# Optimization experiments

Hardware: AMD Instinct MI355X
Metric: run time of the kernel (lower is better)

The kernel has to match this reference:

```python
import jax, jax.numpy as jnp
import numpy as np

D_MODEL, D_STATE, D_CONV, EXPAND = 1024, 16, 4, 2
D_INNER = EXPAND * D_MODEL
B, L = 4, 2048


def setup_inputs() -> dict:
    key = jax.random.key(0)
    ks = jax.random.split(key, 9)
    s = lambda fan_in: 1.0 / np.sqrt(fan_in)
    x = jax.random.normal(ks[0], (B, L, D_MODEL), dtype=jnp.float32)
    W_in = jax.random.normal(ks[1], (D_MODEL, 2 * D_INNER), dtype=jnp.float32) * s(D_MODEL)
    conv_w = jax.random.normal(ks[2], (D_INNER, 1, D_CONV), dtype=jnp.float32) * s(D_CONV)
    conv_b = jax.random.normal(ks[3], (D_INNER,), dtype=jnp.float32) * 0.01
    W_x = jax.random.normal(ks[4], (D_INNER, 2 * D_STATE + 1), dtype=jnp.float32) * s(D_INNER)
    W_dt = jax.random.normal(ks[5], (1, D_INNER), dtype=jnp.float32)
    b_dt = jax.random.normal(ks[6], (D_INNER,), dtype=jnp.float32) * 0.01
    A_log = jnp.log(jnp.tile(jnp.arange(1, D_STATE + 1, dtype=jnp.float32), (D_INNER, 1)))
    D_param = jnp.ones((D_INNER,), dtype=jnp.float32)
    W_out = jax.random.normal(ks[7], (D_INNER, D_MODEL), dtype=jnp.float32) * s(D_INNER)
    return {"x": x, "W_in": W_in, "conv_w": conv_w, "conv_b": conv_b, "W_x": W_x,
            "W_dt": W_dt, "b_dt": b_dt, "A_log": A_log, "D_param": D_param, "W_out": W_out}


def _mamba_forward(x, W_in, conv_w, conv_b, W_x, W_dt, b_dt, A_log, D_param, W_out):
    b, l, _ = x.shape
    xz = x @ W_in                      # [B,L,2*D_INNER]
    x_in, z = jnp.split(xz, 2, axis=-1)
    # causal depthwise conv1d (padding=d_conv-1 on the left, trimmed to L)
    xc = jnp.transpose(x_in, (0, 2, 1))  # [B,C,L]
    xc = jax.lax.conv_general_dilated(
        xc, conv_w, window_strides=(1,), padding=[(D_CONV - 1, 0)],
        dimension_numbers=("NCH", "OIH", "NCH"), feature_group_count=D_INNER)
    xc = xc + conv_b[None, :, None]
    x_conv = jax.nn.silu(jnp.transpose(xc, (0, 2, 1)))  # [B,L,D_INNER]

    xp = x_conv @ W_x                  # [B,L,1+2*D_STATE]
    delta1, B_mat, C_mat = jnp.split(xp, [1, 1 + D_STATE], axis=-1)
    delta = jax.nn.softplus(delta1 @ W_dt + b_dt)       # [B,L,D_INNER]
    A = -jnp.exp(A_log)                # [D_INNER,D_STATE]

    # selective scan over time
    def step(h, inp):
        d_t, B_t, C_t, x_t = inp       # [B,Di], [B,Ds], [B,Ds], [B,Di]
        A_bar = jnp.exp(d_t[:, :, None] * A)                       # [B,Di,Ds]
        h = A_bar * h + (d_t * x_t)[:, :, None] * B_t[:, None, :]  # [B,Di,Ds]
        y = jnp.einsum("bds,bs->bd", h, C_t)                        # [B,Di]
        return h, y

    h0 = jnp.zeros((b, D_INNER, D_STATE), dtype=x.dtype)
    tm = lambda a: jnp.transpose(a, (1, 0, 2))  # time-major
    _, ys = jax.lax.scan(step, h0, (tm(delta), tm(B_mat), tm(C_mat), tm(x_conv)))
    y = jnp.transpose(ys, (1, 0, 2))   # [B,L,D_INNER]

    y = y + x_conv * D_param
    y = y * jax.nn.silu(z)
    return y @ W_out                   # [B,L,D_MODEL]


def reference(x, W_in, conv_w, conv_b, W_x, W_dt, b_dt, A_log, D_param, W_out):
    return _mamba_forward(x, W_in, conv_w, conv_b, W_x, W_dt, b_dt, A_log, D_param, W_out)
```

## Files before the change

kernel.cpp:

```cpp
#include <hip/hip_runtime.h>
#include <hip/hip_bf16.h>
#include <stdint.h>

#define D_STATE 16
#define D_INNER 2048
#define BB 4
#define LL 2048
#define NTOK (BB*LL)
#define NCH 32
#define CHUNK (LL/NCH)
#define XPW 48
#define SCAN_TPB 128

typedef __attribute__((ext_vector_type(8))) short short8;
typedef __attribute__((ext_vector_type(8))) unsigned short u16x8;
typedef __attribute__((ext_vector_type(4))) float f32x4;
typedef __attribute__((ext_vector_type(2))) float f32x2;

__device__ __forceinline__ float b2f(__hip_bfloat16 v) { return __bfloat162float(v); }
__device__ __forceinline__ float ub2f(unsigned short u) {
  unsigned v = (unsigned)u << 16; float f; __builtin_memcpy(&f, &v, 4); return f;
}

__device__ __forceinline__ void g2lds16(const void* g, void* l) {
  __builtin_amdgcn_global_load_lds(
      (const __attribute__((address_space(1))) unsigned*)(uintptr_t)g,
      (__attribute__((address_space(3))) unsigned*)(unsigned)(uintptr_t)l,
      16, 0, 0);
}

__device__ __forceinline__ void store_c(float* p, float v) { *p = v; }
__device__ __forceinline__ void store_c(__hip_bfloat16* p, float v) { *p = __float2bfloat16(v); }

#define PREP_B0 8192
#define PREP_B1 (PREP_B0 + 4096)
#define PREP_B2 (PREP_B1 + 2048)
#define PREP_B3 (PREP_B2 + 384)
__global__ __launch_bounds__(256) void prep_kernel(
    const float* __restrict__ x, __hip_bfloat16* __restrict__ xb,
    const float* __restrict__ W_in, __hip_bfloat16* __restrict__ WT_in,
    const float* __restrict__ W_out, __hip_bfloat16* __restrict__ WT_out,
    const float* __restrict__ W_x, __hip_bfloat16* __restrict__ WTx)
{
  __shared__ float tile[32][33];
  const int bx = blockIdx.x, tid = threadIdx.x;
  if (bx < PREP_B0) {
    int i = bx * 256 + tid;
    const float4 v = ((const float4*)x)[i];
    __hip_bfloat16 o[4] = { __float2bfloat16(v.x), __float2bfloat16(v.y),
                            __float2bfloat16(v.z), __float2bfloat16(v.w) };
    ((ulong1*)xb)[i] = *(ulong1*)o;
  } else if (bx < PREP_B2) {
    const float* in; __hip_bfloat16* out; int R, C, tc, tr;
    if (bx < PREP_B1) {
      int tb = bx - PREP_B0; in = W_in; out = WT_in; R = 1024; C = 4096;
      tc = (tb & 127) * 32; tr = (tb >> 7) * 32;
    } else {
      int tb = bx - PREP_B1; in = W_out; out = WT_out; R = 2048; C = 1024;
      tc = (tb & 31) * 32; tr = (tb >> 5) * 32;
    }
    const int lx = tid & 31, ly = tid >> 5;
    #pragma unroll
    for (int i = 0; i < 32; i += 8)
      tile[ly + i][lx] = in[(size_t)(tr + ly + i) * C + tc + lx];
    __syncthreads();
    #pragma unroll
    for (int i = 0; i < 32; i += 8)
      out[(size_t)(tc + ly + i) * R + tr + lx] = __float2bfloat16(tile[lx][ly + i]);
  } else {
    int idx = (bx - PREP_B2) * 256 + tid;
    int n = idx >> 11, k = idx & 2047;
    int src = (n == 0) ? 0 : ((n >= 2 && n <= 33) ? n - 1 : -1);
    float v = (src >= 0) ? W_x[k * 33 + src] : 0.f;
    WTx[idx] = __float2bfloat16(v);
  }
}

__global__ __launch_bounds__(512, 2) void gemm_bt_256(
    const short* __restrict__ A, const short* __restrict__ BT,
    __hip_bfloat16* __restrict__ C)
{
  constexpr int K = 1024, Nstride = 4096, nk = K >> 5;
  __shared__ alignas(16) short As[4][256 * 32];
  __shared__ alignas(16) short Bs[4][256 * 32];
  const int tid = threadIdx.x;
  const int lane = tid & 63, wid = tid >> 6;
  const int wm = wid & 1, wn = wid >> 1;
  const int lrow = lane & 15, lq = lane >> 4;

  const int wg = blockIdx.x;
  const int xcd = wg & 7, j = wg >> 3;
  const int jm = j >> 2, jn = j & 3;
  const int m0 = ((xcd >> 2) * 16 + jm) * 256;
  const int n0 = ((xcd & 3) * 4 + jn) * 256;

  const int i0 = tid, i1 = tid + 512;
  const int r0 = i0 >> 2, r1 = i1 >> 2;
  const int sw0 = ((i0 & 3) ^ ((r0 >> 1) & 3)) * 8;
  const int sw1 = ((i1 & 3) ^ ((r1 >> 1) & 3)) * 8;
  const short* pA0 = A  + (size_t)(m0 + r0) * K + sw0;
  const short* pA1 = A  + (size_t)(m0 + r1) * K + sw1;
  const short* pB0 = BT + (size_t)(n0 + r0) * K + sw0;
  const short* pB1 = BT + (size_t)(n0 + r1) * K + sw1;

  int offA[8], offB[4];
  #pragma unroll
  for (int mi = 0; mi < 8; ++mi) {
    int ra = wm * 128 + mi * 16 + lrow;
    offA[mi] = ra * 32 + (lq ^ ((ra >> 1) & 3)) * 8;
  }
  #pragma unroll
  for (int ni = 0; ni < 4; ++ni) {
    int rb = wn * 64 + ni * 16 + lrow;
    offB[ni] = rb * 32 + (lq ^ ((rb >> 1) & 3)) * 8;
  }

  f32x4 acc[8][4] = {};
  short8 a0[4], b0[4];

  auto stageA = [&](int t) {
    const int k0 = t << 5, slot = t & 3;
    g2lds16(pA0 + k0, &As[slot][i0 * 8]);
    g2lds16(pA1 + k0, &As[slot][i1 * 8]);
  };
  auto stageB = [&](int t) {
    const int k0 = t << 5, slot = t & 3;
    g2lds16(pB0 + k0, &Bs[slot][i0 * 8]);
    g2lds16(pB1 + k0, &Bs[slot][i1 * 8]);
  };

  auto body = [&](int t, bool doStage, bool doAhead, bool vm4, bool doBar) {
    const int slot = t & 3, slot2 = (t + 1) & 3;
    const short* as = &As[slot][0];
    const short* bs = &Bs[slot][0];
    short8 a1[4];
    #pragma unroll
    for (int mi = 0; mi < 4; ++mi) a1[mi] = *(const short8*)(as + offA[4 + mi]);
    if (doStage) stageA(t + 3);
    __builtin_amdgcn_s_setprio(1);
    #pragma unroll
    for (int mi = 0; mi < 4; ++mi)
      #pragma unroll
      for (int ni = 0; ni < 4; ++ni)
        acc[mi][ni] = __builtin_amdgcn_mfma_f32_16x16x32_bf16(
            a0[mi], b0[ni], acc[mi][ni], 0, 0, 0);
    __builtin_amdgcn_s_setprio(0);
    if (doStage) stageB(t + 3);
    short8 an[4], bn[4];
    if (doAhead) {
      const short* as2 = &As[slot2][0];
      const short* bs2 = &Bs[slot2][0];
      #pragma unroll
      for (int mi = 0; mi < 4; ++mi) an[mi] = *(const short8*)(as2 + offA[mi]);
      #pragma unroll
      for (int ni = 0; ni < 4; ++ni) bn[ni] = *(const short8*)(bs2 + offB[ni]);
    }
    __builtin_amdgcn_s_setprio(1);
    #pragma unroll
    for (int mi = 0; mi < 4; ++mi)
      #pragma unroll
      for (int ni = 0; ni < 4; ++ni)
        acc[4 + mi][ni] = __builtin_amdgcn_mfma_f32_16x16x32_bf16(
            a1[mi], b0[ni], acc[4 + mi][ni], 0, 0, 0);
    __builtin_amdgcn_s_setprio(0);
    if (doAhead) {
      #pragma unroll
      for (int i = 0; i < 4; ++i) { a0[i] = an[i]; b0[i] = bn[i]; }
    }
    if (doBar) {
      if (vm4) asm volatile("s_waitcnt vmcnt(4)\n\ts_barrier" ::: "memory");
      else     asm volatile("s_waitcnt vmcnt(0)\n\ts_barrier" ::: "memory");
    }
  };

  stageA(0); stageB(0); stageA(1); stageB(1); stageA(2); stageB(2);
  asm volatile("s_waitcnt vmcnt(4)\n\ts_barrier" ::: "memory");
  #pragma unroll
  for (int mi = 0; mi < 4; ++mi) a0[mi] = *(const short8*)(&As[0][offA[mi]]);
  #pragma unroll
  for (int ni = 0; ni < 4; ++ni) b0[ni] = *(const short8*)(&Bs[0][offB[ni]]);

  #pragma unroll 4
  for (int t = 0; t < nk - 4; ++t)
    body(t, true, true, true, true);
  body(nk - 4, true,  true,  true,  true);
  body(nk - 3, false, true,  false, true);
  body(nk - 2, false, true,  false, false);
  body(nk - 1, false, false, false, false);

  #pragma unroll
  for (int mi = 0; mi < 8; ++mi)
    #pragma unroll
    for (int ni = 0; ni < 4; ++ni) {
      const int col = n0 + wn * 64 + ni * 16 + lrow;
      #pragma unroll
      for (int r = 0; r < 4; ++r) {
        const int rowg = m0 + wm * 128 + mi * 16 + lq * 4 + r;
        C[(size_t)rowg * Nstride + col] = __float2bfloat16(acc[mi][ni][r]);
      }
    }
}

template <typename OT>
__global__ __launch_bounds__(256) void gemm_bt_128(
    const short* __restrict__ A, const short* __restrict__ BT,
    OT* __restrict__ C, int Nstride, int K)
{
  __shared__ alignas(16) short As[2][128 * 32];
  __shared__ alignas(16) short Bs[2][128 * 32];
  const int tid = threadIdx.x;
  const int lane = tid & 63, wid = tid >> 6;
  const int wm = wid & 1, wn = wid >> 1;
  const int lrow = lane & 15, lq = lane >> 4;

  const int wg = blockIdx.x;
  const int xcd = wg & 7, j = wg >> 3;
  const int jm = j >> 3, jn = j & 7;
  const int m0 = (xcd * 8 + jm) * 128;
  const int n0 = jn * 128;

  f32x4 acc[4][4] = {};

  auto stage = [&](int k0, int buf) {
    #pragma unroll
    for (int t = 0; t < 2; ++t) {
      int idx = t * 256 + tid;
      int row = idx >> 2, kq = idx & 3;
      int ksw = (kq ^ ((row >> 1) & 3)) * 8;
      g2lds16(A  + (size_t)(m0 + row) * K + k0 + ksw, &As[buf][idx * 8]);
      g2lds16(BT + (size_t)(n0 + row) * K + k0 + ksw, &Bs[buf][idx * 8]);
    }
  };

  const int nk = K >> 5;
  stage(0, 0);
  for (int ki = 0; ki < nk; ++ki) {
    const int cur = ki & 1;
    if (ki + 1 < nk) {
      stage((ki + 1) << 5, cur ^ 1);
      asm volatile("s_waitcnt vmcnt(4)\n\ts_barrier" ::: "memory");
    } else {
      asm volatile("s_waitcnt vmcnt(0)\n\ts_barrier" ::: "memory");
    }

    short8 af[4], bfr[4];
    #pragma unroll
    for (int i = 0; i < 4; ++i) {
      int ra = wm * 64 + i * 16 + lrow;
      int rb = wn * 64 + i * 16 + lrow;
      af[i]  = *(const short8*)(&As[cur][ra * 32 + (lq ^ ((ra >> 1) & 3)) * 8]);
      bfr[i] = *(const short8*)(&Bs[cur][rb * 32 + (lq ^ ((rb >> 1) & 3)) * 8]);
    }
    #pragma unroll
    for (int mi = 0; mi < 4; ++mi)
      #pragma unroll
      for (int ni = 0; ni < 4; ++ni)
        acc[mi][ni] = __builtin_amdgcn_mfma_f32_16x16x32_bf16(
            af[mi], bfr[ni], acc[mi][ni], 0, 0, 0);
    asm volatile("s_barrier" ::: "memory");
  }

  #pragma unroll
  for (int mi = 0; mi < 4; ++mi)
    #pragma unroll
    for (int ni = 0; ni < 4; ++ni) {
      int col = n0 + wn * 64 + ni * 16 + lrow;
      #pragma unroll
      for (int r = 0; r < 4; ++r) {
        int rowg = m0 + wm * 64 + mi * 16 + lq * 4 + r;
        store_c(&C[(size_t)rowg * Nstride + col], acc[mi][ni][r]);
      }
    }
}

__global__ __launch_bounds__(256) void gemm_xp(
    const short* __restrict__ A, const short* __restrict__ BT,
    float* __restrict__ Cout)
{
  __shared__ alignas(16) short As[2][64 * 32];
  __shared__ alignas(16) short Bs[2][48 * 32];
  const int tid = threadIdx.x;
  const int lane = tid & 63, wid = tid >> 6;
  const int lrow = lane & 15, lq = lane >> 4;
  const int m0 = blockIdx.x * 64;
  const int row = tid >> 2, kq = tid & 3;
  const int ksw = (kq ^ ((row >> 1) & 3)) * 8;
  const short* pA = A  + (size_t)(m0 + row) * 2048 + ksw;
  const short* pB = BT + (size_t)row * 2048 + ksw;

  f32x4 acc[3] = {};

  auto stage = [&](int k0, int buf) {
    g2lds16(pA + k0, &As[buf][tid * 8]);
    if (wid < 3) g2lds16(pB + k0, &Bs[buf][tid * 8]);
  };

  stage(0, 0);
  for (int ki = 0; ki < 64; ++ki) {
    const int cur = ki & 1;
    if (ki < 63) {
      stage((ki + 1) << 5, cur ^ 1);
      if (wid < 3) asm volatile("s_waitcnt vmcnt(2)\n\ts_barrier" ::: "memory");
      else         asm volatile("s_waitcnt vmcnt(1)\n\ts_barrier" ::: "memory");
    } else {
      asm volatile("s_waitcnt vmcnt(0)\n\ts_barrier" ::: "memory");
    }
    int ra = wid * 16 + lrow;
    short8 af = *(const short8*)(&As[cur][ra * 32 + (lq ^ ((ra >> 1) & 3)) * 8]);
    #pragma unroll
    for (int nt = 0; nt < 3; ++nt) {
      int rb = nt * 16 + lrow;
      short8 bfr = *(const short8*)(&Bs[cur][rb * 32 + (lq ^ ((rb >> 1) & 3)) * 8]);
      acc[nt] = __builtin_amdgcn_mfma_f32_16x16x32_bf16(af, bfr, acc[nt], 0, 0, 0);
    }
    asm volatile("s_barrier" ::: "memory");
  }
  #pragma unroll
  for (int nt = 0; nt < 3; ++nt) {
    int col = nt * 16 + lrow;
    #pragma unroll
    for (int r = 0; r < 4; ++r) {
      int rowg = m0 + wid * 16 + lq * 4 + r;
      Cout[(size_t)rowg * XPW + col] = acc[nt][r];
    }
  }
}

__global__ __launch_bounds__(256) void conv_silu(
    const __hip_bfloat16* __restrict__ xz, const float* __restrict__ conv_w,
    const float* __restrict__ conv_b, __hip_bfloat16* __restrict__ x_conv)
{
  const int t0 = (blockIdx.x & 255) * 8;
  const int b  = blockIdx.x >> 8;
  const int d8 = threadIdx.x * 8;

  float cb[8];
  {
    float4 cb0 = *(const float4*)(conv_b + d8);
    float4 cb1 = *(const float4*)(conv_b + d8 + 4);
    cb[0] = cb0.x; cb[1] = cb0.y; cb[2] = cb0.z; cb[3] = cb0.w;
    cb[4] = cb1.x; cb[5] = cb1.y; cb[6] = cb1.z; cb[7] = cb1.w;
  }
  float4 w[8];
  #pragma unroll
  for (int j = 0; j < 8; ++j) w[j] = *(const float4*)(conv_w + (size_t)(d8 + j) * 4);

  u16x8 xv[11];
  #pragma unroll
  for (int k = 0; k < 11; ++k) {
    int tt = t0 - 3 + k;
    if (tt >= 0)
      xv[k] = *(const u16x8*)(xz + (size_t)(b * LL + tt) * 4096 + d8);
    else
      xv[k] = (u16x8){0, 0, 0, 0, 0, 0, 0, 0};
  }

  #pragma unroll
  for (int j = 0; j < 8; ++j) {
    float acc[8];
    #pragma unroll
    for (int c = 0; c < 8; ++c) acc[c] = cb[c];
    #pragma unroll
    for (int k = 0; k < 4; ++k) {
      #pragma unroll
      for (int c = 0; c < 8; ++c) {
        float wk = (k == 0) ? w[c].x : (k == 1) ? w[c].y : (k == 2) ? w[c].z : w[c].w;
        acc[c] = fmaf(wk, ub2f(xv[j + k][c]), acc[c]);
      }
    }
    __hip_bfloat16 o[8];
    #pragma unroll
    for (int c = 0; c < 8; ++c) {
      float r = acc[c] * __builtin_amdgcn_rcpf(1.f + __expf(-acc[c]));
      o[c] = __float2bfloat16(r);
    }
    *(u16x8*)(x_conv + (size_t)(b * LL + t0 + j) * D_INNER + d8) = *(u16x8*)o;
  }
}


__global__ __launch_bounds__(SCAN_TPB) void scan_phase1(
    const float* __restrict__ xp, const __hip_bfloat16* __restrict__ x_conv,
    const float* __restrict__ W_dt, const float* __restrict__ b_dt,
    float* __restrict__ P1b, float* __restrict__ vb)
{
  const int d = blockIdx.x * SCAN_TPB + threadIdx.x;
  const int c = blockIdx.y, b = blockIdx.z;
  const float Wdt = W_dt[d], bdt = b_dt[d];
  f32x2 v[8];
  #pragma unroll
  for (int i = 0; i < 8; ++i) v[i] = (f32x2){0.f, 0.f};
  float P1 = 1.f;
  const int t0 = c * CHUNK;
  for (int tt = 0; tt < CHUNK; ++tt) {
    const size_t row = (size_t)b * LL + t0 + tt;
    const float* xpt = xp + row * XPW;
    float u = fmaf(xpt[0], Wdt, bdt);
    float e = __expf(u);
    float r = __builtin_amdgcn_rcpf(1.f + e);
    float delta = (u > 20.f) ? u : __logf(1.f + e);
    float du = delta * b2f(x_conv[row * D_INNER + d]);
    float rr = r * r;
    f32x2 a   = {r, rr};
    f32x2 rr2 = {rr, rr};
    f32x2 du2 = {du, du};
    #pragma unroll
    for (int i = 0; i < 8; ++i) {
      f32x2 B2 = *(const f32x2*)(xpt + 2 + 2 * i);
      v[i] = a * v[i] + du2 * B2;
      a = a * rr2;
    }
    P1 *= r;
  }
  const size_t vbase = (size_t)(b * NCH + c) * (D_STATE * D_INNER) + d;
  #pragma unroll
  for (int i = 0; i < 8; ++i) {
    vb[vbase + (size_t)(2 * i)     * D_INNER] = v[i].x;
    vb[vbase + (size_t)(2 * i + 1) * D_INNER] = v[i].y;
  }
  P1b[((size_t)(b * NCH + c) << 11) + d] = P1;
}

__global__ __launch_bounds__(256) void scan_phase2(
    const float* __restrict__ P1b, float* __restrict__ vb)
{
  const int idx = blockIdx.x * 256 + threadIdx.x;
  const int b = idx >> 14, r2 = idx & 16383;
  const int s = r2 >> 10, d2 = r2 & 1023;
  f32x2 h = {0.f, 0.f};
  for (int c = 0; c < NCH; ++c) {
    f32x2 P1 = *(const f32x2*)(P1b + (((size_t)(b * NCH + c)) << 11) + d2 * 2);
    f32x2 P = P1;
    for (int j = 0; j < s; ++j) P *= P1;
    float* vp = vb + (((size_t)(b * NCH + c)) << 15) + (s << 11) + d2 * 2;
    f32x2 v = *(const f32x2*)vp;
    *(f32x2*)vp = h;
    h = P * h + v;
  }
}

__global__ __launch_bounds__(SCAN_TPB) void scan_phase3(
    const float* __restrict__ xp, const __hip_bfloat16* __restrict__ x_conv,
    const __hip_bfloat16* __restrict__ xz,
    const float* __restrict__ W_dt, const float* __restrict__ b_dt,
    const float* __restrict__ D_param,
    const float* __restrict__ hb, __hip_bfloat16* __restrict__ yout)
{
  const int d = blockIdx.x * SCAN_TPB + threadIdx.x;
  const int c = blockIdx.y, b = blockIdx.z;
  const float Wdt = W_dt[d], bdt = b_dt[d];
  const float Dp = D_param[d];
  f32x2 h[8];
  const size_t base = (size_t)(b * NCH + c) * (D_STATE * D_INNER) + d;
  #pragma unroll
  for (int i = 0; i < 8; ++i) {
    h[i].x = hb[base + (size_t)(2 * i)     * D_INNER];
    h[i].y = hb[base + (size_t)(2 * i + 1) * D_INNER];
  }
  const int t0 = c * CHUNK;
  for (int tt = 0; tt < CHUNK; ++tt) {
    const size_t row = (size_t)b * LL + t0 + tt;
    const float* xpt = xp + row * XPW;
    float u = fmaf(xpt[0], Wdt, bdt);
    float e = __expf(u);
    float r = __builtin_amdgcn_rcpf(1.f + e);
    float delta = (u > 20.f) ? u : __logf(1.f + e);
    float xt = b2f(x_conv[row * D_INNER + d]);
    float du = delta * xt;
    float rr = r * r;
    f32x2 a   = {r, rr};
    f32x2 rr2 = {rr, rr};
    f32x2 du2 = {du, du};
    f32x2 y2  = {0.f, 0.f};
    #pragma unroll
    for (int i = 0; i < 8; ++i) {
      f32x2 B2 = *(const f32x2*)(xpt + 2 + 2 * i);
      f32x2 C2 = *(const f32x2*)(xpt + 18 + 2 * i);
      h[i] = a * h[i] + du2 * B2;
      y2 = h[i] * C2 + y2;
      a = a * rr2;
    }
    float y = y2.x + y2.y + xt * Dp;
    float z = b2f(xz[row * 4096 + D_INNER + d]);
    y *= z * __builtin_amdgcn_rcpf(1.f + __expf(-z));
    yout[row * D_INNER + d] = __float2bfloat16(y);
  }
}

extern "C" void kernel_launch(void* const* d_in, const int* in_sizes, int n_in,
                              void* d_out, int out_size, void* d_ws, size_t ws_size,
                              hipStream_t stream) {
  const float* x      = (const float*)d_in[0];
  const float* W_in   = (const float*)d_in[1];
  const float* conv_w = (const float*)d_in[2];
  const float* conv_b = (const float*)d_in[3];
  const float* W_x    = (const float*)d_in[4];
  const float* W_dt   = (const float*)d_in[5];
  const float* b_dt   = (const float*)d_in[6];
  const float* D_par  = (const float*)d_in[8];
  const float* W_out  = (const float*)d_in[9];
  float* out = (float*)d_out;

  char* ws = (char*)d_ws;
  size_t off = 0;
  auto alloc = [&](size_t bytes) -> void* {
    void* p = ws + off; off += (bytes + 255) & ~(size_t)255; return p;
  };
  const size_t SCANB = (size_t)BB * NCH * D_STATE * D_INNER * 4;
  const size_t R1B   = (size_t)NTOK * D_INNER * 2;

  char* R1 = (char*)alloc(R1B);
  __hip_bfloat16* xb    = (__hip_bfloat16*)R1;
  __hip_bfloat16* WT_in = (__hip_bfloat16*)(R1 + (size_t)NTOK * 1024 * 2);
  float* P1b = (float*)R1;
  __hip_bfloat16* y_ws = (__hip_bfloat16*)R1;
  char* R2 = (char*)alloc(SCANB);
  float* vb = (float*)R2;

  __hip_bfloat16* xz     = (__hip_bfloat16*)alloc((size_t)NTOK * 4096 * 2);
  __hip_bfloat16* x_conv = (__hip_bfloat16*)alloc((size_t)NTOK * D_INNER * 2);
  __hip_bfloat16* WT_out = (__hip_bfloat16*)alloc((size_t)1024 * 2048 * 2);
  __hip_bfloat16* WT_x   = (__hip_bfloat16*)alloc((size_t)XPW * 2048 * 2);
  float* xp = (float*)alloc((size_t)NTOK * XPW * 4);
  (void)ws_size; (void)in_sizes; (void)n_in; (void)out_size;

  prep_kernel<<<PREP_B3, 256, 0, stream>>>(x, xb, W_in, WT_in, W_out, WT_out, W_x, WT_x);
  gemm_bt_256<<<512, 512, 0, stream>>>(
      (const short*)xb, (const short*)WT_in, xz);
  conv_silu<<<NTOK / 8, 256, 0, stream>>>(xz, conv_w, conv_b, x_conv);
  gemm_xp<<<NTOK / 64, 256, 0, stream>>>((const short*)x_conv, (const short*)WT_x, xp);
  scan_phase1<<<dim3(D_INNER / SCAN_TPB, NCH, BB), SCAN_TPB, 0, stream>>>(
      xp, x_conv, W_dt, b_dt, P1b, vb);
  scan_phase2<<<(BB * D_STATE * D_INNER / 2) / 256, 256, 0, stream>>>(P1b, vb);
  scan_phase3<<<dim3(D_INNER / SCAN_TPB, NCH, BB), SCAN_TPB, 0, stream>>>(
      xp, x_conv, xz, W_dt, b_dt, D_par, vb, y_ws);
  gemm_bt_128<float><<<512, 256, 0, stream>>>(
      (const short*)y_ws, (const short*)WT_out, out, 1024, 2048);
}
```

Measured before the change: 364.8 us.

## Shrink input GEMM tiles to 256x128 with 3-stage pipeline and higher occupancy

```diff
diff --git a/kernel.cpp b/kernel.cpp
--- a/kernel.cpp
+++ b/kernel.cpp
@@ -76,37 +76,36 @@
   }
 }
 
-__global__ __launch_bounds__(512, 2) void gemm_bt_256(
+__global__ __launch_bounds__(512, 4) void gemm_bt_w(
     const short* __restrict__ A, const short* __restrict__ BT,
     __hip_bfloat16* __restrict__ C)
 {
   constexpr int K = 1024, Nstride = 4096, nk = K >> 5;
-  __shared__ alignas(16) short As[4][256 * 32];
-  __shared__ alignas(16) short Bs[4][256 * 32];
+  __shared__ alignas(16) short As[3][256 * 32];
+  __shared__ alignas(16) short Bs[3][128 * 32];
   const int tid = threadIdx.x;
   const int lane = tid & 63, wid = tid >> 6;
-  const int wm = wid & 1, wn = wid >> 1;
+  const int wm = wid & 3, wn = wid >> 2;
   const int lrow = lane & 15, lq = lane >> 4;
 
   const int wg = blockIdx.x;
   const int xcd = wg & 7, j = wg >> 3;
-  const int jm = j >> 2, jn = j & 3;
+  const int jm = j >> 3, jn = j & 7;
   const int m0 = ((xcd >> 2) * 16 + jm) * 256;
-  const int n0 = ((xcd & 3) * 4 + jn) * 256;
-
-  const int i0 = tid, i1 = tid + 512;
-  const int r0 = i0 >> 2, r1 = i1 >> 2;
-  const int sw0 = ((i0 & 3) ^ ((r0 >> 1) & 3)) * 8;
-  const int sw1 = ((i1 & 3) ^ ((r1 >> 1) & 3)) * 8;
-  const short* pA0 = A  + (size_t)(m0 + r0) * K + sw0;
-  const short* pA1 = A  + (size_t)(m0 + r1) * K + sw1;
-  const short* pB0 = BT + (size_t)(n0 + r0) * K + sw0;
-  const short* pB1 = BT + (size_t)(n0 + r1) * K + sw1;
-
-  int offA[8], offB[4];
-  #pragma unroll
-  for (int mi = 0; mi < 8; ++mi) {
-    int ra = wm * 128 + mi * 16 + lrow;
+  const int n0 = ((xcd & 3) * 8 + jn) * 128;
+
+  const int row0 = tid >> 2, kq = tid & 3;
+  const int row1 = (tid + 512) >> 2;
+  const int sw0 = (kq ^ ((row0 >> 1) & 3)) * 8;
+  const int sw1 = (kq ^ ((row1 >> 1) & 3)) * 8;
+  const short* pA0 = A  + (size_t)(m0 + row0) * K + sw0;
+  const short* pA1 = A  + (size_t)(m0 + row1) * K + sw1;
+  const short* pB0 = BT + (size_t)(n0 + row0) * K + sw0;
+
+  int offA[4], offB[4];
+  #pragma unroll
+  for (int mi = 0; mi < 4; ++mi) {
+    int ra = wm * 64 + mi * 16 + lrow;
     offA[mi] = ra * 32 + (lq ^ ((ra >> 1) & 3)) * 8;
   }
   #pragma unroll
@@ -115,87 +114,56 @@
     offB[ni] = rb * 32 + (lq ^ ((rb >> 1) & 3)) * 8;
   }
 
-  f32x4 acc[8][4] = {};
-  short8 a0[4], b0[4];
-
-  auto stageA = [&](int t) {
-    const int k0 = t << 5, slot = t & 3;
-    g2lds16(pA0 + k0, &As[slot][i0 * 8]);
-    g2lds16(pA1 + k0, &As[slot][i1 * 8]);
+  f32x4 acc[4][4] = {};
+
+  auto stage = [&](int t) {
+    const int k0 = t << 5, slot = t % 3;
+    g2lds16(pA0 + k0, &As[slot][tid * 8]);
+    g2lds16(pA1 + k0, &As[slot][(tid + 512) * 8]);
+    g2lds16(pB0 + k0, &Bs[slot][tid * 8]);
   };
-  auto stageB = [&](int t) {
-    const int k0 = t << 5, slot = t & 3;
-    g2lds16(pB0 + k0, &Bs[slot][i0 * 8]);
-    g2lds16(pB1 + k0, &Bs[slot][i1 * 8]);
-  };
-
-  auto body = [&](int t, bool doStage, bool doAhead, bool vm4, bool doBar) {
-    const int slot = t & 3, slot2 = (t + 1) & 3;
+
+  auto body = [&](int t, bool doStage, int endmode) {
+    const int slot = t % 3;
     const short* as = &As[slot][0];
     const short* bs = &Bs[slot][0];
-    short8 a1[4];
-    #pragma unroll
-    for (int mi = 0; mi < 4; ++mi) a1[mi] = *(const short8*)(as + offA[4 + mi]);
-    if (doStage) stageA(t + 3);
+    short8 af[4], bf[4];
+    #pragma unroll
+    for (int mi = 0; mi < 4; ++mi) af[mi] = *(const short8*)(as + offA[mi]);
+    #pragma unroll
+    for (int ni = 0; ni < 4; ++ni) bf[ni] = *(const short8*)(bs + offB[ni]);
+    if (doStage) stage(t + 2);
     __builtin_amdgcn_s_setprio(1);
     #pragma unroll
     for (int mi = 0; mi < 4; ++mi)
       #pragma unroll
       for (int ni = 0; ni < 4; ++ni)
         acc[mi][ni] = __builtin_amdgcn_mfma_f32_16x16x32_bf16(
-            a0[mi], b0[ni], acc[mi][ni], 0, 0, 0);
+            af[mi], bf[ni], acc[mi][ni], 0, 0, 0);
     __builtin_amdgcn_s_setprio(0);
-    if (doStage) stageB(t + 3);
-    short8 an[4], bn[4];
-    if (doAhead) {
-      const short* as2 = &As[slot2][0];
-      const short* bs2 = &Bs[slot2][0];
-      #pragma unroll
-      for (int mi = 0; mi < 4; ++mi) an[mi] = *(const short8*)(as2 + offA[mi]);
-      #pragma unroll
-      for (int ni = 0; ni < 4; ++ni) bn[ni] = *(const short8*)(bs2 + offB[ni]);
-    }
-    __builtin_amdgcn_s_setprio(1);
-    #pragma unroll
-    for (int mi = 0; mi < 4; ++mi)
-      #pragma unroll
-      for (int ni = 0; ni < 4; ++ni)
-        acc[4 + mi][ni] = __builtin_amdgcn_mfma_f32_16x16x32_bf16(
-            a1[mi], b0[ni], acc[4 + mi][ni], 0, 0, 0);
-    __builtin_amdgcn_s_setprio(0);
-    if (doAhead) {
-      #pragma unroll
-      for (int i = 0; i < 4; ++i) { a0[i] = an[i]; b0[i] = bn[i]; }
-    }
-    if (doBar) {
-      if (vm4) asm volatile("s_waitcnt vmcnt(4)\n\ts_barrier" ::: "memory");
-      else     asm volatile("s_waitcnt vmcnt(0)\n\ts_barrier" ::: "memory");
-    }
+    if (endmode == 3)
+      asm volatile("s_waitcnt vmcnt(3)\n\ts_barrier" ::: "memory");
+    else if (endmode == 0)
+      asm volatile("s_waitcnt vmcnt(0)\n\ts_barrier" ::: "memory");
   };
 
-  stageA(0); stageB(0); stageA(1); stageB(1); stageA(2); stageB(2);
-  asm volatile("s_waitcnt vmcnt(4)\n\ts_barrier" ::: "memory");
-  #pragma unroll
-  for (int mi = 0; mi < 4; ++mi) a0[mi] = *(const short8*)(&As[0][offA[mi]]);
-  #pragma unroll
-  for (int ni = 0; ni < 4; ++ni) b0[ni] = *(const short8*)(&Bs[0][offB[ni]]);
-
-  #pragma unroll 4
-  for (int t = 0; t < nk - 4; ++t)
-    body(t, true, true, true, true);
-  body(nk - 4, true,  true,  true,  true);
-  body(nk - 3, false, true,  false, true);
-  body(nk - 2, false, true,  false, false);
-  body(nk - 1, false, false, false, false);
-
-  #pragma unroll
-  for (int mi = 0; mi < 8; ++mi)
+  stage(0); stage(1);
+  asm volatile("s_waitcnt vmcnt(0)\n\ts_barrier" ::: "memory");
+
+  #pragma unroll 3
+  for (int t = 0; t < nk - 2; ++t)
+    body(t, true, 3);
+  body(nk - 2, false, 0);
+  body(nk - 1, false, -1);
+
+  #pragma unroll
+  for (int mi = 0; mi < 4; ++mi)
     #pragma unroll
     for (int ni = 0; ni < 4; ++ni) {
       const int col = n0 + wn * 64 + ni * 16 + lrow;
       #pragma unroll
       for (int r = 0; r < 4; ++r) {
-        const int rowg = m0 + wm * 128 + mi * 16 + lq * 4 + r;
+        const int rowg = m0 + wm * 64 + mi * 16 + lq * 4 + r;
         C[(size_t)rowg * Nstride + col] = __float2bfloat16(acc[mi][ni][r]);
       }
     }
@@ -525,7 +493,7 @@
   (void)ws_size; (void)in_sizes; (void)n_in; (void)out_size;
 
   prep_kernel<<<PREP_B3, 256, 0, stream>>>(x, xb, W_in, WT_in, W_out, WT_out, W_x, WT_x);
-  gemm_bt_256<<<512, 512, 0, stream>>>(
+  gemm_bt_w<<<1024, 512, 0, stream>>>(
       (const short*)xb, (const short*)WT_in, xz);
   conv_silu<<<NTOK / 8, 256, 0, stream>>>(xz, conv_w, conv_b, x_conv);
   gemm_xp<<<NTOK / 64, 256, 0, stream>>>((const short*)x_conv, (const short*)WT_x, xp);
```

Result: no change. 371.8 us (+1.9%).

## Rewrite output GEMM with 256x128 tiles and 4-stage LDS pipeline

Applied to the files above, without the earlier changes.

```diff
diff --git a/kernel.cpp b/kernel.cpp
--- a/kernel.cpp
+++ b/kernel.cpp
@@ -28,9 +28,6 @@
       (__attribute__((address_space(3))) unsigned*)(unsigned)(uintptr_t)l,
       16, 0, 0);
 }
-
-__device__ __forceinline__ void store_c(float* p, float v) { *p = v; }
-__device__ __forceinline__ void store_c(__hip_bfloat16* p, float v) { *p = __float2bfloat16(v); }
 
 #define PREP_B0 8192
 #define PREP_B1 (PREP_B0 + 4096)
@@ -201,74 +198,107 @@
     }
 }
 
-template <typename OT>
-__global__ __launch_bounds__(256) void gemm_bt_128(
+__global__ __launch_bounds__(512, 2) void gemm_out(
     const short* __restrict__ A, const short* __restrict__ BT,
-    OT* __restrict__ C, int Nstride, int K)
-{
-  __shared__ alignas(16) short As[2][128 * 32];
-  __shared__ alignas(16) short Bs[2][128 * 32];
+    float* __restrict__ C)
+{
+  constexpr int K = 2048, Nstride = 1024, nk = K >> 5;
+  __shared__ alignas(16) short As[4][256 * 32];
+  __shared__ alignas(16) short Bs[4][128 * 32];
   const int tid = threadIdx.x;
   const int lane = tid & 63, wid = tid >> 6;
-  const int wm = wid & 1, wn = wid >> 1;
+  const int wm = wid & 3, wn = wid >> 2;
   const int lrow = lane & 15, lq = lane >> 4;
 
   const int wg = blockIdx.x;
   const int xcd = wg & 7, j = wg >> 3;
   const int jm = j >> 3, jn = j & 7;
-  const int m0 = (xcd * 8 + jm) * 128;
+  const int m0 = (xcd * 4 + jm) * 256;
   const int n0 = jn * 128;
 
+  const int r0 = tid >> 2, r1 = (tid + 512) >> 2, kq = tid & 3;
+  const int sw0 = (kq ^ ((r0 >> 1) & 3)) * 8;
+  const int sw1 = (kq ^ ((r1 >> 1) & 3)) * 8;
+  const short* pA0 = A  + (size_t)(m0 + r0) * K + sw0;
+  const short* pA1 = A  + (size_t)(m0 + r1) * K + sw1;
+  const short* pB0 = BT + (size_t)(n0 + r0) * K + sw0;
+
+  int offA[4], offB[4];
+  #pragma unroll
+  for (int mi = 0; mi < 4; ++mi) {
+    int ra = wm * 64 + mi * 16 + lrow;
+    offA[mi] = ra * 32 + (lq ^ ((ra >> 1) & 3)) * 8;
+  }
+  #pragma unroll
+  for (int ni = 0; ni < 4; ++ni) {
+    int rb = wn * 64 + ni * 16 + lrow;
+    offB[ni] = rb * 32 + (lq ^ ((rb >> 1) & 3)) * 8;
+  }
+
   f32x4 acc[4][4] = {};
-
-  auto stage = [&](int k0, int buf) {
-    #pragma unroll
-    for (int t = 0; t < 2; ++t) {
-      int idx = t * 256 + tid;
-      int row = idx >> 2, kq = idx & 3;
-      int ksw = (kq ^ ((row >> 1) & 3)) * 8;
-      g2lds16(A  + (size_t)(m0 + row) * K + k0 + ksw, &As[buf][idx * 8]);
-      g2lds16(BT + (size_t)(n0 + row) * K + k0 + ksw, &Bs[buf][idx * 8]);
-    }
-  };
-
-  const int nk = K >> 5;
-  stage(0, 0);
-  for (int ki = 0; ki < nk; ++ki) {
-    const int cur = ki & 1;
-    if (ki + 1 < nk) {
-      stage((ki + 1) << 5, cur ^ 1);
-      asm volatile("s_waitcnt vmcnt(4)\n\ts_barrier" ::: "memory");
-    } else {
-      asm volatile("s_waitcnt vmcnt(0)\n\ts_barrier" ::: "memory");
-    }
-
-    short8 af[4], bfr[4];
-    #pragma unroll
-    for (int i = 0; i < 4; ++i) {
-      int ra = wm * 64 + i * 16 + lrow;
-      int rb = wn * 64 + i * 16 + lrow;
-      af[i]  = *(const short8*)(&As[cur][ra * 32 + (lq ^ ((ra >> 1) & 3)) * 8]);
-      bfr[i] = *(const short8*)(&Bs[cur][rb * 32 + (lq ^ ((rb >> 1) & 3)) * 8]);
-    }
+  short8 a0[4], b0[4];
+
+  auto stage = [&](int t) {
+    const int k0 = t << 5, slot = t & 3;
+    g2lds16(pA0 + k0, &As[slot][tid * 8]);
+    g2lds16(pA1 + k0, &As[slot][(tid + 512) * 8]);
+    g2lds16(pB0 + k0, &Bs[slot][tid * 8]);
+  };
+
+  auto body = [&](int t, bool doStage, bool doAhead, bool vm3, bool doBar) {
+    const int slot2 = (t + 1) & 3;
+    short8 an[4], bn[4];
+    if (doAhead) {
+      const short* as2 = &As[slot2][0];
+      const short* bs2 = &Bs[slot2][0];
+      #pragma unroll
+      for (int mi = 0; mi < 4; ++mi) an[mi] = *(const short8*)(as2 + offA[mi]);
+      #pragma unroll
+      for (int ni = 0; ni < 4; ++ni) bn[ni] = *(const short8*)(bs2 + offB[ni]);
+    }
+    if (doStage) stage(t + 3);
+    __builtin_amdgcn_s_setprio(1);
     #pragma unroll
     for (int mi = 0; mi < 4; ++mi)
       #pragma unroll
       for (int ni = 0; ni < 4; ++ni)
         acc[mi][ni] = __builtin_amdgcn_mfma_f32_16x16x32_bf16(
-            af[mi], bfr[ni], acc[mi][ni], 0, 0, 0);
-    asm volatile("s_barrier" ::: "memory");
-  }
+            a0[mi], b0[ni], acc[mi][ni], 0, 0, 0);
+    __builtin_amdgcn_s_setprio(0);
+    if (doAhead) {
+      #pragma unroll
+      for (int i = 0; i < 4; ++i) { a0[i] = an[i]; b0[i] = bn[i]; }
+    }
+    if (doBar) {
+      if (vm3) asm volatile("s_waitcnt vmcnt(3)\n\ts_barrier" ::: "memory");
+      else     asm volatile("s_waitcnt vmcnt(0)\n\ts_barrier" ::: "memory");
+    }
+  };
+
+  stage(0); stage(1); stage(2);
+  asm volatile("s_waitcnt vmcnt(3)\n\ts_barrier" ::: "memory");
+  #pragma unroll
+  for (int mi = 0; mi < 4; ++mi) a0[mi] = *(const short8*)(&As[0][offA[mi]]);
+  #pragma unroll
+  for (int ni = 0; ni < 4; ++ni) b0[ni] = *(const short8*)(&Bs[0][offB[ni]]);
+
+  #pragma unroll 4
+  for (int t = 0; t < nk - 4; ++t)
+    body(t, true, true, true, true);
+  body(nk - 4, true,  true,  true,  true);
+  body(nk - 3, false, true,  false, true);
+  body(nk - 2, false, true,  false, false);
+  body(nk - 1, false, false, false, false);
 
   #pragma unroll
   for (int mi = 0; mi < 4; ++mi)
     #pragma unroll
     for (int ni = 0; ni < 4; ++ni) {
-      int col = n0 + wn * 64 + ni * 16 + lrow;
+      const int col = n0 + wn * 64 + ni * 16 + lrow;
       #pragma unroll
       for (int r = 0; r < 4; ++r) {
-        int rowg = m0 + wm * 64 + mi * 16 + lq * 4 + r;
-        store_c(&C[(size_t)rowg * Nstride + col], acc[mi][ni][r]);
+        const int rowg = m0 + wm * 64 + mi * 16 + lq * 4 + r;
+        C[(size_t)rowg * Nstride + col] = acc[mi][ni][r];
       }
     }
 }
@@ -534,6 +564,6 @@
   scan_phase2<<<(BB * D_STATE * D_INNER / 2) / 256, 256, 0, stream>>>(P1b, vb);
   scan_phase3<<<dim3(D_INNER / SCAN_TPB, NCH, BB), SCAN_TPB, 0, stream>>>(
       xp, x_conv, xz, W_dt, b_dt, D_par, vb, y_ws);
-  gemm_bt_128<float><<<512, 256, 0, stream>>>(
-      (const short*)y_ws, (const short*)WT_out, out, 1024, 2048);
-}
+  gemm_out<<<256, 512, 0, stream>>>(
+      (const short*)y_ws, (const short*)WT_out, out);
+}
```

Measured after the change: 366.4 us. Within noise of the previous version (+0.4%).
